# Kernel optimization log

Hardware: AMD Instinct MI355X
Metric: run time of the kernel (lower is better)

The kernel has to match this reference:

```python
import jax, jax.numpy as jnp
import numpy as np

NUM_NODE = 64   # number of FPS nodes
NSAMPLE = 64    # ball-query / knn group size
RADIUS = 0.3    # first ball-query radius
K_INTERP = 3    # knn for upsample interpolation
BN_EPS = 1e-5


def sqdist(a, b):
    # a [B,S,3], b [B,N,3] -> squared distances [B,S,N]
    return (jnp.sum(a * a, -1)[:, :, None] + jnp.sum(b * b, -1)[:, None, :]
            - 2.0 * jnp.einsum('bsc,bnc->bsn', a, b))


def index_points(points, idx):
    # points [B,C,N] or [B,C,N,1]; idx [B,...] -> gathered [B,C,...]
    if points.ndim == 4:
        points = points[..., 0]
    return jax.vmap(lambda p, i: p[:, i])(points, idx)


def farthest_point_sample(xyz, npoint):
    # xyz [B,3,N] -> idx [B,npoint]; deterministic start at index 0
    B, C, N = xyz.shape

    def body(carry, _):
        dist, far = carry
        centroid = jnp.take_along_axis(xyz, far[:, None, None], axis=2)  # [B,3,1]
        d = jnp.sum((xyz - centroid) ** 2, axis=1)                       # [B,N]
        dist = jnp.minimum(dist, d)
        nxt = jnp.argmax(dist, axis=-1)
        return (dist, nxt), far

    init = (jnp.full((B, N), 1e10, xyz.dtype), jnp.zeros((B,), jnp.int32))
    _, idxs = jax.lax.scan(body, init, None, length=npoint)
    return idxs.T  # [B,npoint]


def query_ball_point(radius, nsample, xyz, new_xyz):
    # xyz [B,3,N], new_xyz [B,3,S] -> group idx [B,S,nsample]
    N = xyz.shape[2]
    sqr = sqdist(jnp.transpose(new_xyz, (0, 2, 1)), jnp.transpose(xyz, (0, 2, 1)))  # [B,S,N]
    if radius is not None:
        idx = jnp.broadcast_to(jnp.arange(N, dtype=jnp.int32), sqr.shape)
        idx = jnp.where(sqr > radius * radius, N, idx)
        idx = jnp.sort(idx, axis=-1)[:, :, :nsample]
        first = idx[:, :, :1]
        idx = jnp.where(idx == N, first, idx)  # pad misses with first hit
    else:
        idx = jnp.argsort(sqr, axis=-1)[:, :, :nsample].astype(jnp.int32)  # knn
    return idx


def _forward(input_fea, input_loc, pred_w, res_w, res_b, bn_gamma, bn_beta):
    # input_fea [B,C,N,1], input_loc [B,3,N]
    fidx = farthest_point_sample(input_loc, NUM_NODE)        # [B,S]
    fpoint_loc = index_points(input_loc, fidx)               # [B,3,S]
    fpoint_fea = index_points(input_fea, fidx)               # [B,C,S]

    gidx = query_ball_point(RADIUS, NSAMPLE, input_loc, fpoint_loc)  # [B,S,K]
    group_fea = index_points(input_fea, gidx) - fpoint_fea[..., None]  # [B,C,S,K]

    # pred_offset: 1x1 conv (no bias) + tanh
    seman = jnp.tanh(jnp.einsum('oc,bcsk->bosk', pred_w, group_fea))  # [B,3,S,K]

    group_loc = index_points(input_loc, gidx) - fpoint_loc[..., None]  # [B,3,S,K]
    node_offset = jnp.mean(seman * group_loc, axis=-1)       # [B,3,S]
    node_loc = fpoint_loc + node_offset                      # [B,3,S]

    gidx2 = query_ball_point(None, NSAMPLE, input_loc, node_loc)  # knn, [B,S,K]

    # residual branch: 1x1 conv + BatchNorm (training-mode batch stats) + ReLU
    res = jnp.einsum('oc,bcnk->bonk', res_w, input_fea) + res_b[None, :, None, None]
    mean = jnp.mean(res, axis=(0, 2, 3), keepdims=True)
    var = jnp.var(res, axis=(0, 2, 3), keepdims=True)
    res = (res - mean) * jax.lax.rsqrt(var + BN_EPS)
    res = jax.nn.relu(res * bn_gamma[None, :, None, None] + bn_beta[None, :, None, None])

    group_res = index_points(res, gidx2)                     # [B,F,S,K]
    node_fea = jnp.max(group_res, axis=-1, keepdims=True)    # [B,F,S,1]

    # upsample_inter: inverse-distance weighted 3-NN interpolation back to N points
    d = sqdist(jnp.transpose(input_loc, (0, 2, 1)), jnp.transpose(node_loc, (0, 2, 1)))  # [B,N,S]
    neg_d, kidx = jax.lax.top_k(-d, K_INTERP)                # k smallest dists
    dists = jnp.maximum(-neg_d, 1e-10)                       # [B,N,k]
    w = 1.0 / dists
    w = w / jnp.sum(w, axis=-1, keepdims=True)               # [B,N,k]
    interp = jnp.sum(index_points(node_fea, kidx) * w[:, None], axis=-1)  # [B,F,N]

    output_fea = jnp.concatenate([input_fea[..., 0], interp], axis=1)[..., None]  # [B,C+F,N,1]
    return output_fea, node_fea, node_offset


def setup_inputs() -> dict:
    key = jax.random.key(0)
    k1, k2, k3, k4, k5 = jax.random.split(key, 5)
    B, C, N = 32, 64, 8192
    FC = 64
    input_fea = jax.random.normal(k1, (B, C, N, 1), dtype=jnp.float32)
    input_loc = jax.random.uniform(k2, (B, 3, N), dtype=jnp.float32)
    pred_w = jax.random.normal(k3, (3, C), dtype=jnp.float32) * (1.0 / np.sqrt(C))
    res_w = jax.random.normal(k4, (FC, C), dtype=jnp.float32) * (1.0 / np.sqrt(C))
    res_b = jnp.zeros((FC,), dtype=jnp.float32)
    bn_gamma = jnp.ones((FC,), dtype=jnp.float32)
    bn_beta = jnp.zeros((FC,), dtype=jnp.float32)
    return {"input_fea": input_fea, "input_loc": input_loc, "pred_w": pred_w,
            "res_w": res_w, "res_b": res_b, "bn_gamma": bn_gamma, "bn_beta": bn_beta}


def reference(input_fea, input_loc, pred_w, res_w, res_b, bn_gamma, bn_beta):
    return _forward(input_fea, input_loc, pred_w, res_w, res_b, bn_gamma, bn_beta)
```

## Files before the change

### kernel.cpp

```cpp
#include <hip/hip_runtime.h>
#include <math.h>

#define BB 32
#define NN 8192
#define CC 64
#define SS 64
#define KK 64

#define WS_FIDX   0
#define WS_NLOC   270336
#define WS_GIDX2  276480
#define WS_PART   407552
#define WS_TOT    2537472
#define WS_SCALE  2541632
#define WS_SHIFT  2541696


__device__ __forceinline__ void fps_body(int b, const float* __restrict__ loc,
                                         int* __restrict__ fidx,
                                         float (*wrv)[8], int (*wri)[8],
                                         float (*wrx)[8], float (*wry)[8],
                                         float (*wrz)[8]) {
#pragma clang fp contract(off)
  __builtin_amdgcn_s_setprio(1);
  int t = threadIdx.x;
  const float* lb = loc + (size_t)b * 3 * NN;
  float px[16], py[16], pz[16], dist[16];
#pragma unroll
  for (int k = 0; k < 16; k++) {
    int p = t + 512 * k;
    px[k] = lb[p];
    py[k] = lb[NN + p];
    pz[k] = lb[2 * NN + p];
    dist[k] = 1e10f;
  }
  int lane = t & 63, w = t >> 6;
  int far = 0;
  float cx = lb[0], cy = lb[NN], cz = lb[2 * NN];
  for (int it = 0; it < 64; it++) {
    if (t == 0) fidx[b * 64 + it] = far;
    float bv = -1.0f; int bi = 0;
    float bx = 0.f, by = 0.f, bz = 0.f;
#pragma unroll
    for (int k = 0; k < 16; k++) {
      float dx = px[k] - cx, dy = py[k] - cy, dz = pz[k] - cz;
      float d = (dx * dx + dy * dy) + dz * dz;
      float dm = dist[k];
      dm = d < dm ? d : dm;
      dist[k] = dm;
      if (dm > bv) { bv = dm; bi = t + 512 * k; bx = px[k]; by = py[k]; bz = pz[k]; }
    }
    float v = bv; int vi = bi;
    float vx = bx, vy = by, vz = bz;
#pragma unroll
    for (int off = 1; off < 64; off <<= 1) {
      float v2 = __shfl_xor(v, off, 64);
      int   i2 = __shfl_xor(vi, off, 64);
      float x2 = __shfl_xor(vx, off, 64);
      float y2 = __shfl_xor(vy, off, 64);
      float z2 = __shfl_xor(vz, off, 64);
      if (v2 > v || (v2 == v && i2 < vi)) { v = v2; vi = i2; vx = x2; vy = y2; vz = z2; }
    }
    int par = it & 1;
    if (lane == 0) {
      wrv[par][w] = v; wri[par][w] = vi;
      wrx[par][w] = vx; wry[par][w] = vy; wrz[par][w] = vz;
    }
    __syncthreads();
    float gv = wrv[par][0]; int gi = wri[par][0];
    float gx = wrx[par][0], gy = wry[par][0], gz = wrz[par][0];
#pragma unroll
    for (int w2 = 1; w2 < 8; w2++) {
      float v2 = wrv[par][w2]; int i2 = wri[par][w2];
      if (v2 > gv || (v2 == gv && i2 < gi)) {
        gv = v2; gi = i2;
        gx = wrx[par][w2]; gy = wry[par][w2]; gz = wrz[par][w2];
      }
    }
    far = gi;
    cx = gx; cy = gy; cz = gz;
  }
}

__device__ __forceinline__ void transpose_body(int tb, const float* __restrict__ fea,
                                               float* __restrict__ feaT, float* tile) {
  int b = tb >> 7;
  int n0 = (tb & 127) * 64;
  int t = threadIdx.x;
  const float* fb = fea + (size_t)b * (CC * NN);
#pragma unroll
  for (int m = 0; m < 8; m++) {
    int idx = m * 512 + t;
    int c = idx >> 6, nl = idx & 63;
    tile[c * 65 + nl] = fb[(size_t)c * NN + n0 + nl];
  }
  __syncthreads();
  float* ob = feaT + ((size_t)b * NN + n0) * 64;
#pragma unroll
  for (int m = 0; m < 8; m++) {
    int idx = m * 512 + t;
    int nl = idx >> 6, c = idx & 63;
    ob[idx] = tile[c * 65 + nl];
  }
}

__device__ __forceinline__ void cov_body(int cb, const float* __restrict__ fea,
                                         float* __restrict__ part,
                                         float* Sf, float* red) {
  int t = threadIdx.x, w = t >> 6, lane = t & 63;
  int i = lane >> 3, j = lane & 7;
  float acc[8][8];
  float rs[8];
#pragma unroll
  for (int r = 0; r < 8; r++) {
    rs[r] = 0.f;
#pragma unroll
    for (int r2 = 0; r2 < 8; r2++) acc[r][r2] = 0.f;
  }
  for (int q = 0; q < 4; q++) {
    int chunk = cb * 4 + q;
    int p0 = chunk * 128;
    int b = p0 >> 13, n0 = p0 & 8191;
    __syncthreads();
    const float* fb = fea + (size_t)b * (CC * NN) + n0;
    for (int m = 0; m < 16; m++) {
      int idx = m * 512 + t;
      int c = idx >> 7, pt = idx & 127;
      Sf[c * 133 + pt] = fb[(size_t)c * NN + pt];
    }
    __syncthreads();
    if (w < 4) {
      for (int pt = w * 32; pt < w * 32 + 32; pt++) {
        float a[8], bv[8];
#pragma unroll
        for (int r = 0; r < 8; r++) {
          a[r] = Sf[(8 * i + r) * 133 + pt];
          bv[r] = Sf[(8 * j + r) * 133 + pt];
        }
#pragma unroll
        for (int r = 0; r < 8; r++) {
          rs[r] += a[r];
#pragma unroll
          for (int r2 = 0; r2 < 8; r2++) acc[r][r2] = fmaf(a[r], bv[r2], acc[r][r2]);
        }
      }
    }
  }
  for (int ww = 0; ww < 4; ww++) {
    if (w == ww) {
#pragma unroll
      for (int r = 0; r < 8; r++) {
#pragma unroll
        for (int r2 = 0; r2 < 8; r2++) {
          int idx = (8 * i + r) * 64 + 8 * j + r2;
          if (ww == 0) red[idx] = acc[r][r2]; else red[idx] += acc[r][r2];
        }
        if (j == 0) {
          int ridx = 4096 + 8 * i + r;
          if (ww == 0) red[ridx] = rs[r]; else red[ridx] += rs[r];
        }
      }
    }
    __syncthreads();
  }
  float* pb = part + (size_t)cb * 4160;
  for (int idx = t; idx < 4160; idx += 512) pb[idx] = red[idx];
}

__global__ __launch_bounds__(512, 1) void phase1_kernel(const float* __restrict__ fea,
                                                        const float* __restrict__ loc,
                                                        float* __restrict__ feaT,
                                                        int* __restrict__ fidx,
                                                        float* __restrict__ part) {
  __shared__ __align__(16) char smem[50688];
  __shared__ float wrv[2][8], wrx[2][8], wry[2][8], wrz[2][8];
  __shared__ int wri[2][8];
  int blk = blockIdx.x;
  if (blk < 32) {
    fps_body(blk, loc, fidx, wrv, wri, wrx, wry, wrz);
  } else if (blk < 4128) {
    transpose_body(blk - 32, fea, feaT, (float*)smem);
  } else {
    cov_body(blk - 4128, fea, part, (float*)smem, (float*)(smem + 34048));
  }
}

__global__ __launch_bounds__(256) void mega_kernel(const float* __restrict__ loc,
                                                   const float* __restrict__ feaT,
                                                   const float* __restrict__ pw,
                                                   const int* __restrict__ fidx,
                                                   const float* __restrict__ part,
                                                   float* __restrict__ tot,
                                                   int* __restrict__ gidx2,
                                                   float* __restrict__ out_noff,
                                                   float* __restrict__ nloc) {
#pragma clang fp contract(off)
  int blk = blockIdx.x;
  if (blk >= 2048) {
    int e = (blk - 2048) * 256 + threadIdx.x;
    if (e < 4160) {
      float sum = 0.f;
      for (int b2 = 0; b2 < 512; b2++) sum += part[(size_t)b2 * 4160 + e];
      tot[e] = sum;
    }
    return;
  }
  int bs = blk, b = bs >> 6, s = bs & 63, t = threadIdx.x;
  int lane = t & 63, w = t >> 6;
  __shared__ unsigned long long masks[128];
  __shared__ unsigned hist[4096];
  __shared__ unsigned partl[256];
  __shared__ float sf[64];
  __shared__ float spw[192];
  __shared__ float sl[3];
  __shared__ float sA[3];
  __shared__ int gidxL[64];
  __shared__ unsigned wrk[4];
  __shared__ int wrp[4];
  __shared__ unsigned selk;
  __shared__ int selp;
  __shared__ int sP, sC0, nOut;
  const float* lb = loc + (size_t)b * 3 * NN;

  if (t < 192) spw[t] = pw[t];
  if (w == 0) {
    int g = fidx[bs];
    sf[lane] = feaT[((size_t)b * NN + g) * 64 + lane];
    if (lane < 3) sl[lane] = lb[(size_t)lane * NN + g];
  }
  __syncthreads();

  {
    float ax = sl[0], ay = sl[1], az = sl[2];
    float A = (ax * ax + ay * ay) + az * az;
    for (int cc = 0; cc < 32; cc++) {
      int ch = w * 32 + cc;
      int p = ch * 64 + lane;
      float bx = lb[p], by = lb[NN + p], bz = lb[2 * NN + p];
      float Bn = (bx * bx + by * by) + bz * bz;
      float dot = fmaf(az, bz, fmaf(ay, by, ax * bx));
      float sqr = (A + Bn) - 2.0f * dot;
      bool hit = !(sqr > 0.09f);
      unsigned long long m = __ballot(hit);
      if (lane == 0) masks[ch] = m;
    }
  }
  __syncthreads();

  if (w == 0) {
    int count = 0, firsth = -1;
    for (int ch = 0; ch < 128 && count < 64; ch++) {
      unsigned long long m = masks[ch];
      if (m) {
        if (firsth < 0) firsth = ch * 64 + (int)__ffsll(m) - 1;
        bool hit = (m >> lane) & 1ull;
        int pos = count + (int)__popcll(m & ((1ull << lane) - 1ull));
        if (hit && pos < 64) gidxL[pos] = ch * 64 + lane;
        count += (int)__popcll(m);
      }
    }
    if (count < 64 && lane >= count) gidxL[lane] = firsth;
  }
  __syncthreads();

  if (w == 0) {
    int g = gidxL[lane];
    const float* fT = feaT + ((size_t)b * NN + g) * 64;
    float a0 = 0.f, a1 = 0.f, a2 = 0.f;
#pragma unroll
    for (int c4 = 0; c4 < 16; c4++) {
      float4 f = *(const float4*)(fT + 4 * c4);
      int c = 4 * c4;
      float g0 = f.x - sf[c + 0];
      a0 = fmaf(spw[c + 0], g0, a0); a1 = fmaf(spw[64 + c + 0], g0, a1); a2 = fmaf(spw[128 + c + 0], g0, a2);
      float g1 = f.y - sf[c + 1];
      a0 = fmaf(spw[c + 1], g1, a0); a1 = fmaf(spw[64 + c + 1], g1, a1); a2 = fmaf(spw[128 + c + 1], g1, a2);
      float g2 = f.z - sf[c + 2];
      a0 = fmaf(spw[c + 2], g2, a0); a1 = fmaf(spw[64 + c + 2], g2, a1); a2 = fmaf(spw[128 + c + 2], g2, a2);
      float g3 = f.w - sf[c + 3];
      a0 = fmaf(spw[c + 3], g3, a0); a1 = fmaf(spw[64 + c + 3], g3, a1); a2 = fmaf(spw[128 + c + 3], g3, a2);
    }
    float c0 = tanhf(a0) * (lb[g] - sl[0]);
    float c1 = tanhf(a1) * (lb[NN + g] - sl[1]);
    float c2 = tanhf(a2) * (lb[2 * NN + g] - sl[2]);
#pragma unroll
    for (int off = 32; off; off >>= 1) {
      c0 += __shfl_xor(c0, off, 64);
      c1 += __shfl_xor(c1, off, 64);
      c2 += __shfl_xor(c2, off, 64);
    }
    if (lane == 0) {
      float m0 = c0 * (1.0f / 64), m1 = c1 * (1.0f / 64), m2 = c2 * (1.0f / 64);
      out_noff[b * 192 + s] = m0;
      out_noff[b * 192 + 64 + s] = m1;
      out_noff[b * 192 + 128 + s] = m2;
      float nx = sl[0] + m0, ny = sl[1] + m1, nz = sl[2] + m2;
      nloc[bs * 3 + 0] = nx;
      nloc[bs * 3 + 1] = ny;
      nloc[bs * 3 + 2] = nz;
      sA[0] = nx; sA[1] = ny; sA[2] = nz;
    }
  }
  __syncthreads();

  float ax = sA[0], ay = sA[1], az = sA[2];
  float A = (ax * ax + ay * ay) + az * az;
  for (int m = 0; m < 16; m++) hist[m * 256 + t] = 0u;
  if (t == 0) nOut = 0;
  __syncthreads();
  unsigned mykey[32];
#pragma unroll
  for (int k = 0; k < 32; k++) {
    int p = t + 256 * k;
    float bx = lb[p], by = lb[NN + p], bz = lb[2 * NN + p];
    float Bn = (bx * bx + by * by) + bz * bz;
    float dot = fmaf(az, bz, fmaf(ay, by, ax * bx));
    float d = (A + Bn) - 2.0f * dot;
    unsigned kb = __float_as_uint(d);
    kb = (kb & 0x80000000u) ? ~kb : (kb | 0x80000000u);
    mykey[k] = kb;
    atomicAdd(&hist[kb >> 20], 1u);
  }
  __syncthreads();
  unsigned ps = 0;
#pragma unroll
  for (int m = 0; m < 16; m++) ps += hist[t * 16 + m];
  partl[t] = ps;
  __syncthreads();
  if (t == 0) {
    int cum = 0, seg = 0;
    for (int t2 = 0; t2 < 256; t2++) {
      if (cum + (int)partl[t2] >= 64) { seg = t2; break; }
      cum += (int)partl[t2];
    }
    int P = seg * 16;
    for (;; P++) {
      if (cum + (int)hist[P] >= 64) break;
      cum += (int)hist[P];
    }
    sP = P; sC0 = cum;
  }
  __syncthreads();
  int P = sP, C0 = sC0;
#pragma unroll
  for (int k = 0; k < 32; k++) {
    if ((int)(mykey[k] >> 20) < P) {
      int pos = atomicAdd(&nOut, 1);
      gidx2[bs * 64 + pos] = t + 256 * k;
    }
  }
  int R = 64 - C0;
  unsigned lastk = 0u; int lastp = -1;
  for (int r = 0; r < R; r++) {
    unsigned bk = 0xFFFFFFFFu; int bp = 0x7FFFFFFF;
#pragma unroll
    for (int k = 0; k < 32; k++) {
      unsigned kk = mykey[k];
      if ((int)(kk >> 20) == P) {
        int p = t + 256 * k;
        bool gt = (kk > lastk) || (kk == lastk && p > lastp);
        if (gt && (kk < bk || (kk == bk && p < bp))) { bk = kk; bp = p; }
      }
    }
#pragma unroll
    for (int off = 1; off < 64; off <<= 1) {
      unsigned k2 = __shfl_xor(bk, off, 64);
      int p2 = __shfl_xor(bp, off, 64);
      if (k2 < bk || (k2 == bk && p2 < bp)) { bk = k2; bp = p2; }
    }
    if (lane == 0) { wrk[w] = bk; wrp[w] = bp; }
    __syncthreads();
    if (t == 0) {
      unsigned fk = wrk[0]; int fp = wrp[0];
#pragma unroll
      for (int w2 = 1; w2 < 4; w2++) {
        unsigned k2 = wrk[w2]; int p2 = wrp[w2];
        if (k2 < fk || (k2 == fk && p2 < fp)) { fk = k2; fp = p2; }
      }
      gidx2[bs * 64 + C0 + r] = fp;
      selk = fk; selp = fp;
    }
    __syncthreads();
    lastk = selk; lastp = selp;
  }
}

__global__ __launch_bounds__(64) void bnstats_kernel(const float* __restrict__ tot,
                                                     const float* __restrict__ rw,
                                                     const float* __restrict__ rb,
                                                     const float* __restrict__ gam,
                                                     const float* __restrict__ bet,
                                                     float* __restrict__ bnsc,
                                                     float* __restrict__ bnsh) {
  int o = threadIdx.x;
  const float invM = 1.0f / 262144.0f;
  float mu = 0.f;
  for (int c = 0; c < 64; c++) mu += rw[o * 64 + c] * (tot[4096 + c] * invM);
  float exx = 0.f;
  for (int c = 0; c < 64; c++) {
    const float* row = tot + c * 64;
    float p = 0.f;
    for (int c2 = 0; c2 < 64; c2++) p += rw[o * 64 + c2] * row[c2];
    exx += rw[o * 64 + c] * p;
  }
  exx *= invM;
  float var = exx - mu * mu;
  float mean = mu + rb[o];
  float sc = gam[o] / sqrtf(var + 1e-5f);
  bnsc[o] = sc;
  bnsh[o] = bet[o] - mean * sc;
}

__global__ __launch_bounds__(256) void nodefea_kernel(const float* __restrict__ feaT,
                                                      const float* __restrict__ rw,
                                                      const int* __restrict__ gidx2,
                                                      const float* __restrict__ bnsc,
                                                      const float* __restrict__ bnsh,
                                                      float* __restrict__ out_nf) {
  __shared__ __align__(16) float Lf[4096];
  __shared__ float Lw[4096];
  __shared__ int Lg[64];
  __shared__ float red[256];
  int bs = blockIdx.x, b = bs >> 6, s = bs & 63, t = threadIdx.x;
  if (t < 64) Lg[t] = gidx2[bs * 64 + t];
  __syncthreads();
#pragma unroll
  for (int m = 0; m < 4; m++) {
    int idx4 = m * 256 + t;
    int k = idx4 >> 4, c4 = idx4 & 15;
    float4 f = *(const float4*)(feaT + ((size_t)b * NN + Lg[k]) * 64 + 4 * c4);
    *(float4*)&Lf[idx4 * 4] = f;
  }
  for (int m = 0; m < 16; m++) {
    int idx = m * 256 + t;
    Lw[idx] = rw[(idx & 63) * 64 + (idx >> 6)];
  }
  __syncthreads();
  int o = t & 63, wq = t >> 6;
  float wreg[64];
#pragma unroll
  for (int c = 0; c < 64; c++) wreg[c] = Lw[c * 64 + o];
  float sc = bnsc[o], sh = bnsh[o];
  float mx = -1e30f;
  for (int k = wq * 16; k < wq * 16 + 16; k++) {
    float raw = 0.f;
#pragma unroll
    for (int c4 = 0; c4 < 16; c4++) {
      float4 lf = *(const float4*)&Lf[k * 64 + c4 * 4];
      raw = fmaf(wreg[4 * c4 + 0], lf.x, raw);
      raw = fmaf(wreg[4 * c4 + 1], lf.y, raw);
      raw = fmaf(wreg[4 * c4 + 2], lf.z, raw);
      raw = fmaf(wreg[4 * c4 + 3], lf.w, raw);
    }
    float v = raw * sc + sh;
    v = v > 0.f ? v : 0.f;
    mx = v > mx ? v : mx;
  }
  red[wq * 64 + o] = mx;
  __syncthreads();
  if (t < 64) {
    float m0 = red[t], m1 = red[64 + t], m2 = red[128 + t], m3 = red[192 + t];
    float ma = m0 > m1 ? m0 : m1;
    float mb = m2 > m3 ? m2 : m3;
    float m = ma > mb ? ma : mb;
    out_nf[b * 4096 + t * 64 + s] = m;
  }
}

__global__ __launch_bounds__(256) void interp_kernel(const float* __restrict__ fea,
                                                     const float* __restrict__ loc,
                                                     const float* __restrict__ nloc,
                                                     const float* __restrict__ nf,
                                                     float* __restrict__ out) {
#pragma clang fp contract(off)
  int b = blockIdx.y;
  int t = threadIdx.x;
  int n = blockIdx.x * 256 + t;
  __shared__ float snl[192];
  __shared__ float sB[64];
  __shared__ float snf[4096];
  if (t < 192) snl[t] = nloc[b * 192 + t];
  {
    const float* nfb = nf + b * 4096;
#pragma unroll
    for (int m = 0; m < 16; m++) snf[m * 256 + t] = nfb[m * 256 + t];
  }
  __syncthreads();
  if (t < 64) {
    float x = snl[t * 3], y = snl[t * 3 + 1], z = snl[t * 3 + 2];
    sB[t] = (x * x + y * y) + z * z;
  }
  __syncthreads();
  const float* lb = loc + (size_t)b * 3 * NN;
  float px = lb[n], py = lb[NN + n], pz = lb[2 * NN + n];
  float A = (px * px + py * py) + pz * pz;
  float d0 = 1e30f, d1 = 1e30f, d2 = 1e30f;
  int i0 = 0, i1 = 0, i2 = 0;
  for (int s = 0; s < 64; s++) {
    float dot = fmaf(pz, snl[s * 3 + 2], fmaf(py, snl[s * 3 + 1], px * snl[s * 3]));
    float d = (A + sB[s]) - 2.0f * dot;
    if (d < d0) { d2 = d1; i2 = i1; d1 = d0; i1 = i0; d0 = d; i0 = s; }
    else if (d < d1) { d2 = d1; i2 = i1; d1 = d; i1 = s; }
    else if (d < d2) { d2 = d; i2 = s; }
  }
  d0 = d0 > 1e-10f ? d0 : 1e-10f;
  d1 = d1 > 1e-10f ? d1 : 1e-10f;
  d2 = d2 > 1e-10f ? d2 : 1e-10f;
  float r0 = 1.0f / d0, r1 = 1.0f / d1, r2 = 1.0f / d2;
  float rsum = (r0 + r1) + r2;
  float w0 = r0 / rsum, w1 = r1 / rsum, w2 = r2 / rsum;
  const float* fb = fea + (size_t)b * (CC * NN);
  float* ob = out + (size_t)b * (128 * NN);
  for (int o = 0; o < 64; o++) {
    ob[(size_t)o * NN + n] = fb[(size_t)o * NN + n];
    float ip = (snf[o * 64 + i0] * w0 + snf[o * 64 + i1] * w1) + snf[o * 64 + i2] * w2;
    ob[(size_t)(64 + o) * NN + n] = ip;
  }
}

extern "C" void kernel_launch(void* const* d_in, const int* in_sizes, int n_in,
                              void* d_out, int out_size, void* d_ws, size_t ws_size,
                              hipStream_t stream) {
  (void)in_sizes; (void)n_in; (void)out_size; (void)ws_size;
  const float* fea = (const float*)d_in[0];
  const float* loc = (const float*)d_in[1];
  const float* pw  = (const float*)d_in[2];
  const float* rw  = (const float*)d_in[3];
  const float* rb  = (const float*)d_in[4];
  const float* gam = (const float*)d_in[5];
  const float* bet = (const float*)d_in[6];
  float* out = (float*)d_out;
  float* ws = (float*)d_ws;

  int*   fidx  = (int*)(ws + WS_FIDX);
  float* nlocp = ws + WS_NLOC;
  int*   gidx2 = (int*)(ws + WS_GIDX2);
  float* part  = ws + WS_PART;
  float* tot   = ws + WS_TOT;
  float* bnsc  = ws + WS_SCALE;
  float* bnsh  = ws + WS_SHIFT;

  float* feaT     = out;
  float* out_nf   = out + 33554432;
  float* out_noff = out + 33685504;

  phase1_kernel<<<dim3(4640), dim3(512), 0, stream>>>(fea, loc, feaT, fidx, part);
  mega_kernel<<<dim3(2065), dim3(256), 0, stream>>>(loc, feaT, pw, fidx, part, tot,
                                                    gidx2, out_noff, nlocp);
  bnstats_kernel<<<dim3(1), dim3(64), 0, stream>>>(tot, rw, rb, gam, bet, bnsc, bnsh);
  nodefea_kernel<<<dim3(2048), dim3(256), 0, stream>>>(feaT, rw, gidx2, bnsc, bnsh, out_nf);
  interp_kernel<<<dim3(32, 32), dim3(256), 0, stream>>>(fea, loc, nlocp, out_nf, out);
}
```

Measured before the change: 648.1 us.

## Split mega kernel into per-stage kernels and move half the passthrough copy into phase1

Splits the monolithic per-node kernel into separate stages: centroid gather and partial-sum reduction, ball query with one wavefront per node (fused with BN statistics), offset prediction, and knn selection. The ball query now scans with early exit per wavefront instead of having all four waves compute every chunk mask. The passthrough copy of input features into the output is split so phase1 writes batches 16-31 while interp writes batches 0-15, to balance the two kernels. This adds two extra kernel launches and workspace round-trips in exchange for finer-grained parallelism and shorter serial stages.

```diff
diff --git a/kernel.cpp b/kernel.cpp
--- a/kernel.cpp
+++ b/kernel.cpp
@@ -8,6 +8,9 @@
 #define KK 64
 
 #define WS_FIDX   0
+#define WS_FLOC   2048
+#define WS_FFEA   8192
+#define WS_GIDX   139264
 #define WS_NLOC   270336
 #define WS_GIDX2  276480
 #define WS_PART   407552
@@ -83,16 +86,21 @@
 }
 
 __device__ __forceinline__ void transpose_body(int tb, const float* __restrict__ fea,
-                                               float* __restrict__ feaT, float* tile) {
+                                               float* __restrict__ feaT,
+                                               float* __restrict__ out, float* tile) {
   int b = tb >> 7;
   int n0 = (tb & 127) * 64;
   int t = threadIdx.x;
   const float* fb = fea + (size_t)b * (CC * NN);
+  float* pb = out + (size_t)b * (128 * NN);
+  bool pass = (b >= 16);
 #pragma unroll
   for (int m = 0; m < 8; m++) {
     int idx = m * 512 + t;
     int c = idx >> 6, nl = idx & 63;
-    tile[c * 65 + nl] = fb[(size_t)c * NN + n0 + nl];
+    float v = fb[(size_t)c * NN + n0 + nl];
+    tile[c * 65 + nl] = v;
+    if (pass) pb[(size_t)c * NN + n0 + nl] = v;
   }
   __syncthreads();
   float* ob = feaT + ((size_t)b * NN + n0) * 64;
@@ -170,6 +178,7 @@
 __global__ __launch_bounds__(512, 1) void phase1_kernel(const float* __restrict__ fea,
                                                         const float* __restrict__ loc,
                                                         float* __restrict__ feaT,
+                                                        float* __restrict__ out,
                                                         int* __restrict__ fidx,
                                                         float* __restrict__ part) {
   __shared__ __align__(16) char smem[50688];
@@ -179,62 +188,56 @@
   if (blk < 32) {
     fps_body(blk, loc, fidx, wrv, wri, wrx, wry, wrz);
   } else if (blk < 4128) {
-    transpose_body(blk - 32, fea, feaT, (float*)smem);
+    transpose_body(blk - 32, fea, feaT, out, (float*)smem);
   } else {
     cov_body(blk - 4128, fea, part, (float*)smem, (float*)(smem + 34048));
   }
 }
 
-__global__ __launch_bounds__(256) void mega_kernel(const float* __restrict__ loc,
-                                                   const float* __restrict__ feaT,
-                                                   const float* __restrict__ pw,
-                                                   const int* __restrict__ fidx,
-                                                   const float* __restrict__ part,
-                                                   float* __restrict__ tot,
-                                                   int* __restrict__ gidx2,
-                                                   float* __restrict__ out_noff,
-                                                   float* __restrict__ nloc) {
+__global__ __launch_bounds__(256) void phase2_kernel(const float* __restrict__ part,
+                                                     float* __restrict__ tot,
+                                                     const float* __restrict__ loc,
+                                                     const float* __restrict__ fea,
+                                                     const int* __restrict__ fidx,
+                                                     float* __restrict__ floc,
+                                                     float* __restrict__ ffea) {
+  int blk = blockIdx.x, t = threadIdx.x;
+  if (blk < 17) {
+    int e = blk * 256 + t;
+    if (e >= 4160) return;
+    float s = 0.f;
+    for (int b2 = 0; b2 < 512; b2++) s += part[(size_t)b2 * 4160 + e];
+    tot[e] = s;
+  } else {
+    int bs = (blk - 17) * 4 + (t >> 6);
+    int c = t & 63;
+    int b = bs >> 6;
+    int g = fidx[bs];
+    ffea[bs * 64 + c] = fea[(size_t)b * (CC * NN) + (size_t)c * NN + g];
+    if (c < 3) floc[bs * 3 + c] = loc[(size_t)b * (3 * NN) + (size_t)c * NN + g];
+  }
+}
+
+__global__ __launch_bounds__(256) void phase3_kernel(const float* __restrict__ loc,
+                                                     const float* __restrict__ floc,
+                                                     int* __restrict__ gidx,
+                                                     const float* __restrict__ tot,
+                                                     const float* __restrict__ rw,
+                                                     const float* __restrict__ rb,
+                                                     const float* __restrict__ gam,
+                                                     const float* __restrict__ bet,
+                                                     float* __restrict__ bnsc,
+                                                     float* __restrict__ bnsh) {
 #pragma clang fp contract(off)
   int blk = blockIdx.x;
-  if (blk >= 2048) {
-    int e = (blk - 2048) * 256 + threadIdx.x;
-    if (e < 4160) {
-      float sum = 0.f;
-      for (int b2 = 0; b2 < 512; b2++) sum += part[(size_t)b2 * 4160 + e];
-      tot[e] = sum;
-    }
-    return;
-  }
-  int bs = blk, b = bs >> 6, s = bs & 63, t = threadIdx.x;
-  int lane = t & 63, w = t >> 6;
-  __shared__ unsigned long long masks[128];
-  __shared__ unsigned hist[4096];
-  __shared__ unsigned partl[256];
-  __shared__ float sf[64];
-  __shared__ float spw[192];
-  __shared__ float sl[3];
-  __shared__ float sA[3];
-  __shared__ int gidxL[64];
-  __shared__ unsigned wrk[4];
-  __shared__ int wrp[4];
-  __shared__ unsigned selk;
-  __shared__ int selp;
-  __shared__ int sP, sC0, nOut;
-  const float* lb = loc + (size_t)b * 3 * NN;
-
-  if (t < 192) spw[t] = pw[t];
-  if (w == 0) {
-    int g = fidx[bs];
-    sf[lane] = feaT[((size_t)b * NN + g) * 64 + lane];
-    if (lane < 3) sl[lane] = lb[(size_t)lane * NN + g];
-  }
-  __syncthreads();
-
-  {
-    float ax = sl[0], ay = sl[1], az = sl[2];
+  if (blk < 512) {
+    int w = threadIdx.x >> 6, lane = threadIdx.x & 63;
+    int bs = blk * 4 + w, b = bs >> 6;
+    const float* lb = loc + (size_t)b * 3 * NN;
+    float ax = floc[bs * 3], ay = floc[bs * 3 + 1], az = floc[bs * 3 + 2];
     float A = (ax * ax + ay * ay) + az * az;
-    for (int cc = 0; cc < 32; cc++) {
-      int ch = w * 32 + cc;
+    int count = 0, firsth = -1;
+    for (int ch = 0; ch < 128 && count < 64; ch++) {
       int p = ch * 64 + lane;
       float bx = lb[p], by = lb[NN + p], bz = lb[2 * NN + p];
       float Bn = (bx * bx + by * by) + bz * bz;
@@ -242,69 +245,105 @@
       float sqr = (A + Bn) - 2.0f * dot;
       bool hit = !(sqr > 0.09f);
       unsigned long long m = __ballot(hit);
-      if (lane == 0) masks[ch] = m;
-    }
-  }
-  __syncthreads();
-
-  if (w == 0) {
-    int count = 0, firsth = -1;
-    for (int ch = 0; ch < 128 && count < 64; ch++) {
-      unsigned long long m = masks[ch];
       if (m) {
         if (firsth < 0) firsth = ch * 64 + (int)__ffsll(m) - 1;
-        bool hit = (m >> lane) & 1ull;
         int pos = count + (int)__popcll(m & ((1ull << lane) - 1ull));
-        if (hit && pos < 64) gidxL[pos] = ch * 64 + lane;
+        if (hit && pos < 64) gidx[bs * 64 + pos] = p;
         count += (int)__popcll(m);
       }
     }
-    if (count < 64 && lane >= count) gidxL[lane] = firsth;
-  }
-  __syncthreads();
-
-  if (w == 0) {
-    int g = gidxL[lane];
-    const float* fT = feaT + ((size_t)b * NN + g) * 64;
-    float a0 = 0.f, a1 = 0.f, a2 = 0.f;
-#pragma unroll
-    for (int c4 = 0; c4 < 16; c4++) {
-      float4 f = *(const float4*)(fT + 4 * c4);
-      int c = 4 * c4;
-      float g0 = f.x - sf[c + 0];
-      a0 = fmaf(spw[c + 0], g0, a0); a1 = fmaf(spw[64 + c + 0], g0, a1); a2 = fmaf(spw[128 + c + 0], g0, a2);
-      float g1 = f.y - sf[c + 1];
-      a0 = fmaf(spw[c + 1], g1, a0); a1 = fmaf(spw[64 + c + 1], g1, a1); a2 = fmaf(spw[128 + c + 1], g1, a2);
-      float g2 = f.z - sf[c + 2];
-      a0 = fmaf(spw[c + 2], g2, a0); a1 = fmaf(spw[64 + c + 2], g2, a1); a2 = fmaf(spw[128 + c + 2], g2, a2);
-      float g3 = f.w - sf[c + 3];
-      a0 = fmaf(spw[c + 3], g3, a0); a1 = fmaf(spw[64 + c + 3], g3, a1); a2 = fmaf(spw[128 + c + 3], g3, a2);
-    }
-    float c0 = tanhf(a0) * (lb[g] - sl[0]);
-    float c1 = tanhf(a1) * (lb[NN + g] - sl[1]);
-    float c2 = tanhf(a2) * (lb[2 * NN + g] - sl[2]);
-#pragma unroll
-    for (int off = 32; off; off >>= 1) {
-      c0 += __shfl_xor(c0, off, 64);
-      c1 += __shfl_xor(c1, off, 64);
-      c2 += __shfl_xor(c2, off, 64);
-    }
-    if (lane == 0) {
-      float m0 = c0 * (1.0f / 64), m1 = c1 * (1.0f / 64), m2 = c2 * (1.0f / 64);
-      out_noff[b * 192 + s] = m0;
-      out_noff[b * 192 + 64 + s] = m1;
-      out_noff[b * 192 + 128 + s] = m2;
-      float nx = sl[0] + m0, ny = sl[1] + m1, nz = sl[2] + m2;
-      nloc[bs * 3 + 0] = nx;
-      nloc[bs * 3 + 1] = ny;
-      nloc[bs * 3 + 2] = nz;
-      sA[0] = nx; sA[1] = ny; sA[2] = nz;
-    }
-  }
-  __syncthreads();
-
-  float ax = sA[0], ay = sA[1], az = sA[2];
+    if (count < 64 && lane >= count) gidx[bs * 64 + lane] = firsth;
+  } else {
+    int o = threadIdx.x;
+    if (o >= 64) return;
+    const float invM = 1.0f / 262144.0f;
+    float mu = 0.f;
+    for (int c = 0; c < 64; c++) mu += rw[o * 64 + c] * (tot[4096 + c] * invM);
+    float exx = 0.f;
+    for (int c = 0; c < 64; c++) {
+      const float* row = tot + c * 64;
+      float p = 0.f;
+      for (int c2 = 0; c2 < 64; c2++) p += rw[o * 64 + c2] * row[c2];
+      exx += rw[o * 64 + c] * p;
+    }
+    exx *= invM;
+    float var = exx - mu * mu;
+    float mean = mu + rb[o];
+    float sc = gam[o] / sqrtf(var + 1e-5f);
+    bnsc[o] = sc;
+    bnsh[o] = bet[o] - mean * sc;
+  }
+}
+
+__global__ __launch_bounds__(64) void seman_kernel(const float* __restrict__ feaT,
+                                                   const float* __restrict__ loc,
+                                                   const float* __restrict__ pw,
+                                                   const int* __restrict__ gidx,
+                                                   const float* __restrict__ ffea,
+                                                   const float* __restrict__ floc,
+                                                   float* __restrict__ out_noff,
+                                                   float* __restrict__ nloc) {
+  int bs = blockIdx.x, b = bs >> 6, s = bs & 63, k = threadIdx.x;
+  __shared__ float sf[64];
+  __shared__ float spw[192];
+  __shared__ float sl[3];
+  sf[k] = ffea[bs * 64 + k];
+  spw[k] = pw[k]; spw[64 + k] = pw[64 + k]; spw[128 + k] = pw[128 + k];
+  if (k < 3) sl[k] = floc[bs * 3 + k];
+  __syncthreads();
+  int g = gidx[bs * 64 + k];
+  const float* fT = feaT + ((size_t)b * NN + g) * 64;
+  float a0 = 0.f, a1 = 0.f, a2 = 0.f;
+#pragma unroll
+  for (int c4 = 0; c4 < 16; c4++) {
+    float4 f = *(const float4*)(fT + 4 * c4);
+    int c = 4 * c4;
+    float g0 = f.x - sf[c + 0];
+    a0 = fmaf(spw[c + 0], g0, a0); a1 = fmaf(spw[64 + c + 0], g0, a1); a2 = fmaf(spw[128 + c + 0], g0, a2);
+    float g1 = f.y - sf[c + 1];
+    a0 = fmaf(spw[c + 1], g1, a0); a1 = fmaf(spw[64 + c + 1], g1, a1); a2 = fmaf(spw[128 + c + 1], g1, a2);
+    float g2 = f.z - sf[c + 2];
+    a0 = fmaf(spw[c + 2], g2, a0); a1 = fmaf(spw[64 + c + 2], g2, a1); a2 = fmaf(spw[128 + c + 2], g2, a2);
+    float g3 = f.w - sf[c + 3];
+    a0 = fmaf(spw[c + 3], g3, a0); a1 = fmaf(spw[64 + c + 3], g3, a1); a2 = fmaf(spw[128 + c + 3], g3, a2);
+  }
+  const float* lb = loc + (size_t)b * 3 * NN;
+  float c0 = tanhf(a0) * (lb[g] - sl[0]);
+  float c1 = tanhf(a1) * (lb[NN + g] - sl[1]);
+  float c2 = tanhf(a2) * (lb[2 * NN + g] - sl[2]);
+#pragma unroll
+  for (int off = 32; off; off >>= 1) {
+    c0 += __shfl_xor(c0, off, 64);
+    c1 += __shfl_xor(c1, off, 64);
+    c2 += __shfl_xor(c2, off, 64);
+  }
+  if (k == 0) {
+    float m0 = c0 * (1.0f / 64), m1 = c1 * (1.0f / 64), m2 = c2 * (1.0f / 64);
+    out_noff[b * 192 + s] = m0;
+    out_noff[b * 192 + 64 + s] = m1;
+    out_noff[b * 192 + 128 + s] = m2;
+    nloc[bs * 3 + 0] = sl[0] + m0;
+    nloc[bs * 3 + 1] = sl[1] + m1;
+    nloc[bs * 3 + 2] = sl[2] + m2;
+  }
+}
+
+__global__ __launch_bounds__(256) void knn_kernel(const float* __restrict__ loc,
+                                                  const float* __restrict__ nloc,
+                                                  int* __restrict__ gidx2) {
+#pragma clang fp contract(off)
+  int bs = blockIdx.x, b = bs >> 6, t = threadIdx.x;
+  int lane = t & 63, w = t >> 6;
+  const float* lb = loc + (size_t)b * 3 * NN;
+  float ax = nloc[bs * 3], ay = nloc[bs * 3 + 1], az = nloc[bs * 3 + 2];
   float A = (ax * ax + ay * ay) + az * az;
+  __shared__ unsigned hist[4096];
+  __shared__ unsigned partl[256];
+  __shared__ unsigned wrk[4];
+  __shared__ int wrp[4];
+  __shared__ unsigned selk;
+  __shared__ int selp;
+  __shared__ int sP, sC0, nOut;
   for (int m = 0; m < 16; m++) hist[m * 256 + t] = 0u;
   if (t == 0) nOut = 0;
   __syncthreads();
@@ -383,32 +422,6 @@
     __syncthreads();
     lastk = selk; lastp = selp;
   }
-}
-
-__global__ __launch_bounds__(64) void bnstats_kernel(const float* __restrict__ tot,
-                                                     const float* __restrict__ rw,
-                                                     const float* __restrict__ rb,
-                                                     const float* __restrict__ gam,
-                                                     const float* __restrict__ bet,
-                                                     float* __restrict__ bnsc,
-                                                     float* __restrict__ bnsh) {
-  int o = threadIdx.x;
-  const float invM = 1.0f / 262144.0f;
-  float mu = 0.f;
-  for (int c = 0; c < 64; c++) mu += rw[o * 64 + c] * (tot[4096 + c] * invM);
-  float exx = 0.f;
-  for (int c = 0; c < 64; c++) {
-    const float* row = tot + c * 64;
-    float p = 0.f;
-    for (int c2 = 0; c2 < 64; c2++) p += rw[o * 64 + c2] * row[c2];
-    exx += rw[o * 64 + c] * p;
-  }
-  exx *= invM;
-  float var = exx - mu * mu;
-  float mean = mu + rb[o];
-  float sc = gam[o] / sqrtf(var + 1e-5f);
-  bnsc[o] = sc;
-  bnsh[o] = bet[o] - mean * sc;
 }
 
 __global__ __launch_bounds__(256) void nodefea_kernel(const float* __restrict__ feaT,
@@ -511,8 +524,9 @@
   float w0 = r0 / rsum, w1 = r1 / rsum, w2 = r2 / rsum;
   const float* fb = fea + (size_t)b * (CC * NN);
   float* ob = out + (size_t)b * (128 * NN);
+  bool pass = (b < 16);
   for (int o = 0; o < 64; o++) {
-    ob[(size_t)o * NN + n] = fb[(size_t)o * NN + n];
+    if (pass) ob[(size_t)o * NN + n] = fb[(size_t)o * NN + n];
     float ip = (snf[o * 64 + i0] * w0 + snf[o * 64 + i1] * w1) + snf[o * 64 + i2] * w2;
     ob[(size_t)(64 + o) * NN + n] = ip;
   }
@@ -533,6 +547,9 @@
   float* ws = (float*)d_ws;
 
   int*   fidx  = (int*)(ws + WS_FIDX);
+  float* floc  = ws + WS_FLOC;
+  float* ffea  = ws + WS_FFEA;
+  int*   gidx  = (int*)(ws + WS_GIDX);
   float* nlocp = ws + WS_NLOC;
   int*   gidx2 = (int*)(ws + WS_GIDX2);
   float* part  = ws + WS_PART;
@@ -544,10 +561,11 @@
   float* out_nf   = out + 33554432;
   float* out_noff = out + 33685504;
 
-  phase1_kernel<<<dim3(4640), dim3(512), 0, stream>>>(fea, loc, feaT, fidx, part);
-  mega_kernel<<<dim3(2065), dim3(256), 0, stream>>>(loc, feaT, pw, fidx, part, tot,
-                                                    gidx2, out_noff, nlocp);
-  bnstats_kernel<<<dim3(1), dim3(64), 0, stream>>>(tot, rw, rb, gam, bet, bnsc, bnsh);
+  phase1_kernel<<<dim3(4640), dim3(512), 0, stream>>>(fea, loc, feaT, out, fidx, part);
+  phase2_kernel<<<dim3(529), dim3(256), 0, stream>>>(part, tot, loc, fea, fidx, floc, ffea);
+  phase3_kernel<<<dim3(513), dim3(256), 0, stream>>>(loc, floc, gidx, tot, rw, rb, gam, bet, bnsc, bnsh);
+  seman_kernel<<<dim3(2048), dim3(64), 0, stream>>>(feaT, loc, pw, gidx, ffea, floc, out_noff, nlocp);
+  knn_kernel<<<dim3(2048), dim3(256), 0, stream>>>(loc, nlocp, gidx2);
   nodefea_kernel<<<dim3(2048), dim3(256), 0, stream>>>(feaT, rw, gidx2, bnsc, bnsh, out_nf);
   interp_kernel<<<dim3(32, 32), dim3(256), 0, stream>>>(fea, loc, nlocp, out_nf, out);
 }
```

Result: faster. 592.6 us (-8.6%).
